# Optimization experiments

Measured on AMD Instinct MI355X. Metric: run time of the kernel, lower is better.

Reference implementation:

```python
import jax, jax.numpy as jnp
import numpy as np
import math

BN, NA, NE = 8192, 15, 16
DO, DA, DE = 96, 88, 80
H, NH = 512, 8
A_MOVE = 6


def _mha(q_in, kv, mask, Wq, Wk, Wv, Wo, n_heads):
    # q_in: [B,H] single query; kv: [B,L,H]; mask: [B,L] bool (True = valid)
    B, Hd = q_in.shape
    Hh = Hd // n_heads
    q = (q_in @ Wq).reshape(B, n_heads, 1, Hh)
    k = (kv @ Wk).reshape(B, -1, n_heads, Hh).transpose(0, 2, 1, 3)  # [B,nh,L,Hh]
    v = (kv @ Wv).reshape(B, -1, n_heads, Hh).transpose(0, 2, 1, 3)
    scores = jnp.einsum('bhqd,bhkd->bhqk', q, k) / math.sqrt(Hh)
    scores = jnp.where(mask[:, None, None, :], scores, -1e9)
    attn = jax.nn.softmax(scores, axis=-1)
    out = jnp.einsum('bhqk,bhkd->bhqd', attn, v).reshape(B, Hd)
    return out @ Wo


def _gru_cell(x, h, W_ih, W_hh, b_ih, b_hh):
    # torch GRU cell math. x: [B,3H], h: [B,H]
    gi = x @ W_ih.T + b_ih  # [B,3H]
    gh = h @ W_hh.T + b_hh  # [B,3H]
    i_r, i_z, i_n = jnp.split(gi, 3, axis=-1)
    h_r, h_z, h_n = jnp.split(gh, 3, axis=-1)
    r = jax.nn.sigmoid(i_r + h_r)
    z = jax.nn.sigmoid(i_z + h_z)
    n = jnp.tanh(i_n + r * h_n)
    return (1.0 - z) * n + z * h


def setup_inputs() -> dict:
    key = jax.random.key(0)
    ks = jax.random.split(key, 24)
    s = 0.02
    inp = {
        'own': jax.random.normal(ks[0], (BN, 1, DO), jnp.float32),
        'ally': jax.random.normal(ks[1], (BN, NA, DA), jnp.float32),
        'enemy': jax.random.normal(ks[2], (BN, NE, DE), jnp.float32),
        'prev_h': jax.random.normal(ks[3], (BN, H), jnp.float32),
        'W_own': jax.random.normal(ks[4], (DO, H), jnp.float32) * s,
        'b_own': jnp.zeros((H,), jnp.float32),
        'W_ally': jax.random.normal(ks[5], (DA, H), jnp.float32) * s,
        'b_ally': jnp.zeros((H,), jnp.float32),
        'W_enemy': jax.random.normal(ks[6], (DE, H), jnp.float32) * s,
        'b_enemy': jnp.zeros((H,), jnp.float32),
        'Wq_a': jax.random.normal(ks[7], (H, H), jnp.float32) * s,
        'Wk_a': jax.random.normal(ks[8], (H, H), jnp.float32) * s,
        'Wv_a': jax.random.normal(ks[9], (H, H), jnp.float32) * s,
        'Wo_a': jax.random.normal(ks[10], (H, H), jnp.float32) * s,
        'Wq_e': jax.random.normal(ks[11], (H, H), jnp.float32) * s,
        'Wk_e': jax.random.normal(ks[12], (H, H), jnp.float32) * s,
        'Wv_e': jax.random.normal(ks[13], (H, H), jnp.float32) * s,
        'Wo_e': jax.random.normal(ks[14], (H, H), jnp.float32) * s,
        'W_ih': jax.random.normal(ks[15], (3 * H, 3 * H), jnp.float32) * s,
        'W_hh': jax.random.normal(ks[16], (3 * H, H), jnp.float32) * s,
        'b_ih': jnp.zeros((3 * H,), jnp.float32),
        'b_hh': jnp.zeros((3 * H,), jnp.float32),
        'W_q': jax.random.normal(ks[17], (H, A_MOVE + NE), jnp.float32) * s,
        'b_q': jnp.zeros((A_MOVE + NE,), jnp.float32),
    }
    return inp


def reference(own, ally, enemy, prev_h,
              W_own, b_own, W_ally, b_ally, W_enemy, b_enemy,
              Wq_a, Wk_a, Wv_a, Wo_a, Wq_e, Wk_e, Wv_e, Wo_e,
              W_ih, W_hh, b_ih, b_hh, W_q, b_q):
    # masks: entity valid iff not all-zero feature row
    ally_mask = ~jnp.all(ally == 0, axis=-1)    # [B,NA]
    enemy_mask = ~jnp.all(enemy == 0, axis=-1)  # [B,NE]

    e_own = (own @ W_own + b_own)[:, 0, :]      # [B,H]
    A = ally @ W_ally + b_ally                   # [B,NA,H]
    E = enemy @ W_enemy + b_enemy                # [B,NE,H]

    zA = _mha(e_own, A, ally_mask, Wq_a, Wk_a, Wv_a, Wo_a, NH)
    zE = _mha(e_own, E, enemy_mask, Wq_e, Wk_e, Wv_e, Wo_e, NH)

    x = jnp.concatenate([e_own, zA, zE], axis=-1)  # [B,3H]
    h = _gru_cell(x, prev_h, W_ih, W_hh, b_ih, b_hh)
    q = h @ W_q + b_q                              # [B, A_move + NE]
    return q
```

## Files before the change

kernel.cpp:

```cpp
#include <hip/hip_runtime.h>
#include <cstdint>


typedef unsigned short bf16_t;
typedef __attribute__((ext_vector_type(8))) short bf16x8;
typedef __attribute__((ext_vector_type(4))) float f32x4;

__device__ inline float bf2f(bf16_t v) { return __uint_as_float(((unsigned)v) << 16); }
__device__ inline bf16_t f2bf(float x) {
    unsigned u = __float_as_uint(x);
    u += 0x7fffu + ((u >> 16) & 1u);
    return (bf16_t)(u >> 16);
}
__device__ inline void gload16(const bf16_t* g, bf16_t* l) {
    __builtin_amdgcn_global_load_lds(
        (const __attribute__((address_space(1))) void*)g,
        (__attribute__((address_space(3))) void*)l, 16, 0, 0);
}
__device__ inline int imin(int a, int b) { return a < b ? a : b; }

struct CJob { const float* s; bf16_t* d; int n4; };
template <int NJ> struct CJobs { CJob j[NJ]; };

template <int NJ>
__global__ __launch_bounds__(256)
void cvt_plain(CJobs<NJ> T)
{
    CJob jb = T.j[blockIdx.y];
    int stride = gridDim.x * 256;
    for (int i = blockIdx.x * 256 + threadIdx.x; i < jb.n4; i += stride) {
        float4 v = ((const float4*)jb.s)[i];
        ushort4 u; u.x = f2bf(v.x); u.y = f2bf(v.y); u.z = f2bf(v.z); u.w = f2bf(v.w);
        ((ushort4*)jb.d)[i] = u;
    }
}

struct TJob { const float* s; bf16_t* d; int R, C; };
template <int NJ> struct TJobs { TJob j[NJ]; };

template <int NJ>
__global__ __launch_bounds__(256)
void cvt_trans(TJobs<NJ> T)
{
    TJob jb = T.j[blockIdx.z];
    int c0 = blockIdx.x * 32, r0 = blockIdx.y * 32;
    if (c0 >= jb.C || r0 >= jb.R) return;
    __shared__ float t[32][33];
    int tx = threadIdx.x & 31, ty = threadIdx.x >> 5;
    for (int i = ty; i < 32; i += 8) {
        int r = r0 + i, c = c0 + tx;
        t[i][tx] = (r < jb.R && c < jb.C) ? jb.s[(int64_t)r * jb.C + c] : 0.f;
    }
    __syncthreads();
    for (int i = ty; i < 32; i += 8) {
        int c = c0 + i, r = r0 + tx;
        if (c < jb.C && r < jb.R) jb.d[(int64_t)c * jb.R + r] = f2bf(t[tx][i]);
    }
}

struct MJob { const bf16_t* A; const bf16_t* Bm; const float* bias; bf16_t* C;
              int lda, ldb, ldc, M, N, K, c32; };
template <int NJ> struct MJobs { MJob j[NJ]; };

template <int NJ>
__global__ __launch_bounds__(256)
void mfma_multi(MJobs<NJ> T)
{
    const MJob jb = T.j[blockIdx.z];
    const int m0 = blockIdx.x * 64, n0 = blockIdx.y * 64;
    if (m0 >= jb.M || n0 >= jb.N) return;
    __shared__ bf16_t As[64][32];
    __shared__ bf16_t Bs[64][32];
    const int tid = threadIdx.x;
    const int wv = tid >> 6, lane = tid & 63;
    const int fr = lane & 15, fq = lane >> 4;
    const int wm = (wv & 1) * 32, wn = (wv >> 1) * 32;
    const int lrow = tid >> 2;
    const int sw = ((lrow >> 1) & 3) ^ (tid & 3);
    const int ar = imin(m0 + lrow, jb.M - 1);
    const int br = imin(n0 + lrow, jb.N - 1);
    const bf16_t* gA = jb.A + (int64_t)ar * jb.lda + sw * 8;
    const bf16_t* gB = jb.Bm + (int64_t)br * jb.ldb + sw * 8;
    bf16_t* lA = &As[wv * 16][0];
    bf16_t* lB = &Bs[wv * 16][0];
    f32x4 acc[2][2] = {};
    for (int k0 = 0; k0 < jb.K; k0 += 32) {
        gload16(gA, lA);
        gload16(gB, lB);
        gA += 32; gB += 32;
        __syncthreads();
        bf16x8 aF[2], bF[2];
#pragma unroll
        for (int i = 0; i < 2; ++i) {
            int rw = wm + i * 16 + fr;
            aF[i] = *(const bf16x8*)&As[rw][(fq ^ ((rw >> 1) & 3)) * 8];
            int rn = wn + i * 16 + fr;
            bF[i] = *(const bf16x8*)&Bs[rn][(fq ^ ((rn >> 1) & 3)) * 8];
        }
#pragma unroll
        for (int i = 0; i < 2; ++i)
#pragma unroll
            for (int j = 0; j < 2; ++j)
                acc[i][j] = __builtin_amdgcn_mfma_f32_16x16x32_bf16(aF[i], bF[j], acc[i][j], 0, 0, 0);
        __syncthreads();
    }
#pragma unroll
    for (int j = 0; j < 2; ++j) {
        const int col = n0 + wn + j * 16 + fr;
        if (col >= jb.N) continue;
        const float bv = jb.bias ? jb.bias[col] : 0.f;
#pragma unroll
        for (int i = 0; i < 2; ++i) {
            const int rowb = m0 + wm + i * 16 + fq * 4;
#pragma unroll
            for (int r = 0; r < 4; ++r) {
                const int row = rowb + r;
                if (row >= jb.M) continue;
                const float v = acc[i][j][r] + bv;
                if (jb.c32) ((float*)jb.C)[(int64_t)row * jb.ldc + col] = v;
                else jb.C[(int64_t)row * jb.ldc + col] = f2bf(v);
            }
        }
    }
}

__global__ __launch_bounds__(256)
void mfma_nt(const bf16_t* __restrict__ A, int lda,
             const bf16_t* __restrict__ Bm, int ldb,
             bf16_t* __restrict__ C, int ldc,
             const float* __restrict__ bias, int K)
{
    __shared__ bf16_t As[128][32];
    __shared__ bf16_t Bs[128][32];
    const int tid = threadIdx.x;
    const int wv = tid >> 6, lane = tid & 63;
    const int fr = lane & 15, fq = lane >> 4;
    const int m0 = blockIdx.x * 128, n0 = blockIdx.y * 128;
    const int wm = (wv & 1) * 64, wn = (wv >> 1) * 64;
    const int lrow = tid >> 2;
    const int sw = ((lrow >> 1) & 3) ^ (tid & 3);
    f32x4 acc[4][4] = {};
    const bf16_t* gA = A + (int64_t)(m0 + lrow) * lda + sw * 8;
    const bf16_t* gB = Bm + (int64_t)(n0 + lrow) * ldb + sw * 8;
    bf16_t* lA0 = &As[wv * 16][0];
    bf16_t* lA1 = &As[64 + wv * 16][0];
    bf16_t* lB0 = &Bs[wv * 16][0];
    bf16_t* lB1 = &Bs[64 + wv * 16][0];
    const int64_t a64 = (int64_t)64 * lda, b64 = (int64_t)64 * ldb;
    for (int k0 = 0; k0 < K; k0 += 32) {
        gload16(gA, lA0);
        gload16(gA + a64, lA1);
        gload16(gB, lB0);
        gload16(gB + b64, lB1);
        gA += 32; gB += 32;
        __syncthreads();
        bf16x8 aF[4], bF[4];
#pragma unroll
        for (int i = 0; i < 4; ++i) {
            int rw = wm + i * 16 + fr;
            aF[i] = *(const bf16x8*)&As[rw][(fq ^ ((rw >> 1) & 3)) * 8];
            int rn = wn + i * 16 + fr;
            bF[i] = *(const bf16x8*)&Bs[rn][(fq ^ ((rn >> 1) & 3)) * 8];
        }
#pragma unroll
        for (int i = 0; i < 4; ++i)
#pragma unroll
            for (int j = 0; j < 4; ++j)
                acc[i][j] = __builtin_amdgcn_mfma_f32_16x16x32_bf16(aF[i], bF[j], acc[i][j], 0, 0, 0);
        __syncthreads();
    }
#pragma unroll
    for (int j = 0; j < 4; ++j) {
        const int col = n0 + wn + j * 16 + fr;
        const float bv = bias[col];
#pragma unroll
        for (int i = 0; i < 4; ++i) {
            const int row = m0 + wm + i * 16 + fq * 4;
#pragma unroll
            for (int r = 0; r < 4; ++r)
                C[(int64_t)(row + r) * ldc + col] = f2bf(acc[i][j][r] + bv);
        }
    }
}

template <int NENT, int DF, int OFF, bool COPYOWN>
__global__ __launch_bounds__(256)
void attn_mfma(const float* __restrict__ ent, const bf16_t* __restrict__ Kq,
               const bf16_t* __restrict__ ownB, bf16_t* __restrict__ acat)
{
    __shared__ bf16_t sent[4][16][104];
    __shared__ bf16_t sentT[4][96][24];
    __shared__ bf16_t pbuf[4][16][24];
    __shared__ float  maskf[4][16];

    const int wv = threadIdx.x >> 6, lane = threadIdx.x & 63;
    const int b = blockIdx.x * 4 + wv;
    const int fr = lane & 15, g = lane >> 4;
    const bf16x8 z8 = {0, 0, 0, 0, 0, 0, 0, 0};

    if (lane < 16) maskf[wv][lane] = -1e9f;
    const float* eb = ent + (int64_t)b * NENT * DF;
#pragma unroll
    for (int t = 0; t < 3; ++t) {
        int idx = lane + t * 64;
        int i = idx / 12, c0 = (idx % 12) * 8;
        float v[8];
        bool data = (i < NENT) && (c0 < DF);
        if (data) {
            float4 a = *(const float4*)(eb + (int64_t)i * DF + c0);
            float4 c = *(const float4*)(eb + (int64_t)i * DF + c0 + 4);
            v[0] = a.x; v[1] = a.y; v[2] = a.z; v[3] = a.w;
            v[4] = c.x; v[5] = c.y; v[6] = c.z; v[7] = c.w;
        } else {
#pragma unroll
            for (int j = 0; j < 8; ++j) v[j] = 0.f;
        }
        bf16x8 pk;
        bool any = false;
#pragma unroll
        for (int j = 0; j < 8; ++j) { pk[j] = (short)f2bf(v[j]); any = any || (v[j] != 0.f); }
        *(bf16x8*)&sent[wv][i][c0] = pk;
#pragma unroll
        for (int j = 0; j < 8; ++j) sentT[wv][c0 + j][i] = (bf16_t)pk[j];
        if (any) maskf[wv][i] = 0.f;
    }
    __syncthreads();

    const bf16_t* kqr = Kq + (size_t)b * 768 + fr * 96;
    const float biash = (fr < 8) ? bf2f(kqr[DF]) : 0.f;
    f32x4 S = {};
#pragma unroll
    for (int m = 0; m < 3; ++m) {
        int kc = m * 32 + g * 8;
        bf16x8 af = *(const bf16x8*)&sent[wv][fr][kc];
        bf16x8 kf = (fr < 8) ? *(const bf16x8*)(kqr + kc) : z8;
        S = __builtin_amdgcn_mfma_f32_16x16x32_bf16(af, kf, S, 0, 0, 0);
    }
    float4 mk = *(const float4*)&maskf[wv][g * 4];
    float s0 = (S[0] + biash) * 0.125f + mk.x;
    float s1 = (S[1] + biash) * 0.125f + mk.y;
    float s2 = (S[2] + biash) * 0.125f + mk.z;
    float s3 = (S[3] + biash) * 0.125f + mk.w;
    float mx = fmaxf(fmaxf(s0, s1), fmaxf(s2, s3));
    mx = fmaxf(mx, __shfl_xor(mx, 16, 64));
    mx = fmaxf(mx, __shfl_xor(mx, 32, 64));
    float e0 = __expf(s0 - mx), e1 = __expf(s1 - mx);
    float e2 = __expf(s2 - mx), e3 = __expf(s3 - mx);
    float sum = e0 + e1 + e2 + e3;
    sum += __shfl_xor(sum, 16, 64);
    sum += __shfl_xor(sum, 32, 64);
    float inv = 1.f / sum;
    ushort4 pu;
    pu.x = f2bf(e0 * inv); pu.y = f2bf(e1 * inv);
    pu.z = f2bf(e2 * inv); pu.w = f2bf(e3 * inv);
    *(ushort4*)&pbuf[wv][fr][g * 4] = pu;
    __syncthreads();

    bf16x8 pa = (g < 2) ? *(const bf16x8*)&pbuf[wv][fr][g * 8] : z8;
    f32x4 o[6] = {};
#pragma unroll
    for (int t = 0; t < 6; ++t) {
        bf16x8 bfv = (g < 2) ? *(const bf16x8*)&sentT[wv][t * 16 + fr][g * 8] : z8;
        o[t] = __builtin_amdgcn_mfma_f32_16x16x32_bf16(pa, bfv, o[t], 0, 0, 0);
    }
    bf16_t* ob = &sent[wv][0][0];
    if (g < 2) {
#pragma unroll
        for (int t = 0; t < 6; ++t)
#pragma unroll
            for (int r = 0; r < 4; ++r)
                ob[(g * 4 + r) * 96 + t * 16 + fr] = f2bf(o[t][r]);
    }
    __syncthreads();

    bf16_t* arow = acat + (int64_t)b * 1440;
    if (COPYOWN && lane < 12)
        *(bf16x8*)(arow + lane * 8) = *(const bf16x8*)(ownB + (int64_t)b * 96 + lane * 8);
    constexpr int CH = DF / 8;
    if (lane < 8 * CH) {
        int hh = lane / CH, j = lane % CH;
        *(bf16x8*)(arow + OFF + hh * DF + j * 8) = *(const bf16x8*)&ob[hh * 96 + j * 8];
    }
}

__global__ __launch_bounds__(256)
void bias_fuse(const float* __restrict__ b_own, const float* __restrict__ b_ally,
               const float* __restrict__ b_enemy,
               const float* __restrict__ Wq_a, const float* __restrict__ Wq_e,
               const float* __restrict__ Wk_a, const float* __restrict__ Wv_a,
               const float* __restrict__ Wk_e, const float* __restrict__ Wv_e,
               float* __restrict__ fb)
{
    int job = blockIdx.x;
    int n = blockIdx.y * 64 + (threadIdx.x >> 2), q = threadIdx.x & 3;
    const float* v; const float* W;
    switch (job) {
        case 0: v = b_own;   W = Wq_a; break;
        case 1: v = b_own;   W = Wq_e; break;
        case 2: v = b_ally;  W = Wk_a; break;
        case 3: v = b_ally;  W = Wv_a; break;
        case 4: v = b_enemy; W = Wk_e; break;
        default: v = b_enemy; W = Wv_e; break;
    }
    float s = 0.f;
    for (int h = q * 128; h < q * 128 + 128; ++h)
        s = fmaf(v[h], W[(int64_t)h * 512 + n], s);
    s += __shfl_xor(s, 1);
    s += __shfl_xor(s, 2);
    if (q == 0) fb[job * 512 + n] = s;
}

__global__ __launch_bounds__(256)
void fixups(const float* __restrict__ fb, bf16_t* __restrict__ FkAB, bf16_t* __restrict__ FkEB,
            float* __restrict__ b2f, const float* __restrict__ b_ih,
            const float* __restrict__ b_own, const float* __restrict__ W_ih,
            const bf16_t* __restrict__ WfaB, const bf16_t* __restrict__ WfeB,
            float* __restrict__ biasgi)
{
    int blk = blockIdx.x, t = threadIdx.x;
    if (blk < 2) {
        int i = blk * 256 + t;
        FkAB[88 * 512 + i] = f2bf(fb[2 * 512 + i]);
        FkEB[80 * 512 + i] = f2bf(fb[4 * 512 + i]);
    } else if (blk < 8) {
        int idx = (blk - 2) * 256 + t;
        int side = idx / 768, n = idx - side * 768;
        int z = n / 96, c = n - z * 96;
        float s = 0.f;
        if (c < 92) {
            const bf16_t* Fk = side ? FkEB : FkAB;
            const float* bq = fb + side * 512;
            const float* bk = fb + (side ? 4 : 2) * 512;
            int BROW = side ? 80 : 88;
            for (int d = 0; d < 64; ++d) {
                float kv = (c == BROW) ? bk[z * 64 + d] : bf2f(Fk[c * 512 + z * 64 + d]);
                s = fmaf(bq[z * 64 + d], kv, s);
            }
        }
        b2f[idx] = s;
    } else {
        int j = (blk - 8) * 64 + (t >> 2), q = t & 3;
        float s = 0.f;
        for (int k = q * 128; k < q * 128 + 128; ++k) {
            s = fmaf(b_own[k],        W_ih[(int64_t)j * 1536 + k], s);
            s = fmaf(fb[3 * 512 + k], bf2f(WfaB[j * 512 + k]), s);
            s = fmaf(fb[5 * 512 + k], bf2f(WfeB[j * 512 + k]), s);
        }
        s += __shfl_xor(s, 1);
        s += __shfl_xor(s, 2);
        if (q == 0) biasgi[j] = s + b_ih[j];
    }
}

__global__ __launch_bounds__(256)
void gru_final(const bf16_t* __restrict__ gi, const bf16_t* __restrict__ gh,
               const float* __restrict__ ph, const bf16_t* __restrict__ Wq,
               const float* __restrict__ bq, float* __restrict__ out, int B)
{
    const int b = blockIdx.x, tid = threadIdx.x;
    __shared__ float sh[512];
    const bf16_t* gib = gi + (int64_t)b * 1536;
    const bf16_t* ghb = gh + (int64_t)b * 1536;
    const float* phb = ph + (int64_t)b * 512;
    for (int n = tid; n < 512; n += 256) {
        float r = 1.f / (1.f + expf(-(bf2f(gib[n]) + bf2f(ghb[n]))));
        float z = 1.f / (1.f + expf(-(bf2f(gib[512 + n]) + bf2f(ghb[512 + n]))));
        float nn = tanhf(bf2f(gib[1024 + n]) + r * bf2f(ghb[1024 + n]));
        sh[n] = (1.f - z) * nn + z * phb[n];
    }
    __syncthreads();
    if (tid < 176) {
        int j = tid >> 3, l = tid & 7;
        float s = 0.f;
        for (int k = l; k < 512; k += 8) s = fmaf(sh[k], bf2f(Wq[j * 512 + k]), s);
        s += __shfl_down(s, 4, 64);
        s += __shfl_down(s, 2, 64);
        s += __shfl_down(s, 1, 64);
        if (l == 0) out[(int64_t)b * 22 + j] = s + bq[j];
    }
}

extern "C" void kernel_launch(void* const* d_in, const int* in_sizes, int n_in,
                              void* d_out, int out_size, void* d_ws, size_t ws_size,
                              hipStream_t stream)
{
    const float* own    = (const float*)d_in[0];
    const float* ally   = (const float*)d_in[1];
    const float* enemy  = (const float*)d_in[2];
    const float* prev_h = (const float*)d_in[3];
    const float* W_own  = (const float*)d_in[4];
    const float* b_own  = (const float*)d_in[5];
    const float* W_ally = (const float*)d_in[6];
    const float* b_ally = (const float*)d_in[7];
    const float* W_enemy= (const float*)d_in[8];
    const float* b_enemy= (const float*)d_in[9];
    const float* Wq_a   = (const float*)d_in[10];
    const float* Wk_a   = (const float*)d_in[11];
    const float* Wv_a   = (const float*)d_in[12];
    const float* Wo_a   = (const float*)d_in[13];
    const float* Wq_e   = (const float*)d_in[14];
    const float* Wk_e   = (const float*)d_in[15];
    const float* Wv_e   = (const float*)d_in[16];
    const float* Wo_e   = (const float*)d_in[17];
    const float* W_ih   = (const float*)d_in[18];
    const float* W_hh   = (const float*)d_in[19];
    const float* b_ih   = (const float*)d_in[20];
    const float* b_hh   = (const float*)d_in[21];
    const float* W_q    = (const float*)d_in[22];
    const float* b_q    = (const float*)d_in[23];
    float* outq = (float*)d_out;
    (void)n_in; (void)out_size;

    const int B = in_sizes[0] / 96;

    float* w = (float*)d_ws;
    size_t o = 0;
    auto alloc = [&](size_t n) { float* p = w + o; o += (n + 3) & ~(size_t)3; return p; };
    bf16_t* WqT[6];
    for (int i = 0; i < 6; ++i) WqT[i] = (bf16_t*)alloc(131072);
    bf16_t* WoaB  = (bf16_t*)alloc(131072);
    bf16_t* WoeB  = (bf16_t*)alloc(131072);
    bf16_t* WihB  = (bf16_t*)alloc(1179648);
    bf16_t* WhhB  = (bf16_t*)alloc(393216);
    bf16_t* WownB = (bf16_t*)alloc(24576);
    bf16_t* WallyB= (bf16_t*)alloc(22528);
    bf16_t* WenemyB=(bf16_t*)alloc(20480);
    bf16_t* ownB  = (bf16_t*)alloc(393216);
    bf16_t* FqaB  = (bf16_t*)alloc(24576);
    bf16_t* FqeB  = (bf16_t*)alloc(24576);
    bf16_t* FkAB  = (bf16_t*)alloc(23552);
    bf16_t* FkEB  = (bf16_t*)alloc(23552);
    bf16_t* FvAB  = (bf16_t*)alloc(22528);
    bf16_t* FvEB  = (bf16_t*)alloc(20480);
    bf16_t* WfaB  = (bf16_t*)alloc(393216);
    bf16_t* WfeB  = (bf16_t*)alloc(393216);
    bf16_t* MmPa  = (bf16_t*)alloc(36864);
    bf16_t* MmPe  = (bf16_t*)alloc(36864);
    float*  b2f   = alloc(1536);
    float*  fb    = alloc(3072);
    bf16_t* Kq    = (bf16_t*)alloc((size_t)B * 768 / 2);
    bf16_t* prevhB= (bf16_t*)w;
    bf16_t* gi    = (bf16_t*)w;
    if (o < (size_t)B * 1536 / 2) return;
    float*  biasgi= alloc(1536);
    bf16_t* WqTq  = (bf16_t*)alloc(5632);
    bf16_t* UTb   = (bf16_t*)alloc(1105920);
    bf16_t* A_cat = (bf16_t*)alloc((size_t)B * 1440 / 2);
    bf16_t* ghB   = (bf16_t*)alloc((size_t)B * 1536 / 2);

    if (ws_size < o * sizeof(float)) return;

    {
        CJobs<8> T;
        T.j[0] = { W_ih,    WihB,    589824 };
        T.j[1] = { W_hh,    WhhB,    196608 };
        T.j[2] = { Wo_a,    WoaB,     65536 };
        T.j[3] = { Wo_e,    WoeB,     65536 };
        T.j[4] = { W_own,   WownB,    12288 };
        T.j[5] = { W_ally,  WallyB,   11264 };
        T.j[6] = { W_enemy, WenemyB,  10240 };
        T.j[7] = { own,     ownB,    196608 };
        hipLaunchKernelGGL((cvt_plain<8>), dim3(128, 8), dim3(256), 0, stream, T);
    }
    {
        TJobs<7> T;
        T.j[0] = { Wq_a, WqT[0], 512, 512 };
        T.j[1] = { Wq_e, WqT[1], 512, 512 };
        T.j[2] = { Wk_a, WqT[2], 512, 512 };
        T.j[3] = { Wk_e, WqT[3], 512, 512 };
        T.j[4] = { Wv_a, WqT[4], 512, 512 };
        T.j[5] = { Wv_e, WqT[5], 512, 512 };
        T.j[6] = { W_q,  WqTq,   512,  22 };
        hipLaunchKernelGGL((cvt_trans<7>), dim3(16, 16, 7), dim3(256), 0, stream, T);
    }
    hipLaunchKernelGGL(bias_fuse, dim3(6, 8), dim3(256), 0, stream,
                       b_own, b_ally, b_enemy, Wq_a, Wq_e, Wk_a, Wv_a, Wk_e, Wv_e, fb);
    {
        MJobs<8> T;
        T.j[0] = { WownB,        WqT[0], nullptr, FqaB, 512, 512, 512,   96, 512, 512, 0 };
        T.j[1] = { WownB,        WqT[1], nullptr, FqeB, 512, 512, 512,   96, 512, 512, 0 };
        T.j[2] = { WallyB,       WqT[2], nullptr, FkAB, 512, 512, 512,   88, 512, 512, 0 };
        T.j[3] = { WenemyB,      WqT[3], nullptr, FkEB, 512, 512, 512,   80, 512, 512, 0 };
        T.j[4] = { WallyB,       WqT[4], nullptr, FvAB, 512, 512, 512,   88, 512, 512, 0 };
        T.j[5] = { WenemyB,      WqT[5], nullptr, FvEB, 512, 512, 512,   80, 512, 512, 0 };
        T.j[6] = { WihB + 512,   WoaB,   nullptr, WfaB, 1536, 512, 512, 1536, 512, 512, 0 };
        T.j[7] = { WihB + 1024,  WoeB,   nullptr, WfeB, 1536, 512, 512, 1536, 512, 512, 0 };
        hipLaunchKernelGGL((mfma_multi<8>), dim3(24, 8, 8), dim3(256), 0, stream, T);
    }
    hipLaunchKernelGGL(fixups, dim3(32), dim3(256), 0, stream,
                       fb, FkAB, FkEB, b2f, b_ih, b_own, W_ih, WfaB, WfeB, biasgi);
    {
        MJobs<33> T;
        for (int h = 0; h < 8; ++h) {
            T.j[h]     = { FkAB + h * 64, FqaB + h * 64, nullptr, MmPa + h * 9216,
                           512, 512, 96, 92, 96, 64, 0 };
            T.j[8 + h] = { FkEB + h * 64, FqeB + h * 64, nullptr, MmPe + h * 9216,
                           512, 512, 96, 92, 96, 64, 0 };
        }
        T.j[16] = { WihB, WownB, nullptr, UTb, 1536, 512, 1440, 1536, 96, 512, 0 };
        for (int h = 0; h < 8; ++h) {
            T.j[17 + h] = { WfaB + h * 64, FvAB + h * 64, nullptr, UTb + 96 + h * 88,
                            512, 512, 1440, 1536, 88, 64, 0 };
            T.j[25 + h] = { WfeB + h * 64, FvEB + h * 64, nullptr, UTb + 800 + h * 80,
                            512, 512, 1440, 1536, 80, 64, 0 };
        }
        hipLaunchKernelGGL((mfma_multi<33>), dim3(24, 2, 33), dim3(256), 0, stream, T);
    }
    {
        CJobs<1> T;
        T.j[0] = { prev_h, prevhB, B * 512 / 4 };
        hipLaunchKernelGGL((cvt_plain<1>), dim3(512, 1), dim3(256), 0, stream, T);
    }
    hipLaunchKernelGGL(mfma_nt, dim3(B / 128, 12), dim3(256), 0, stream,
                       prevhB, 512, WhhB, 512, ghB, 1536, b_hh, 512);
    hipLaunchKernelGGL(mfma_nt, dim3(B / 128, 6), dim3(256), 0, stream,
                       ownB, 96, MmPa, 96, Kq, 768, b2f, 96);
    hipLaunchKernelGGL((attn_mfma<15, 88, 96, true>), dim3(B / 4), dim3(256), 0, stream,
                       ally, Kq, ownB, A_cat);
    hipLaunchKernelGGL(mfma_nt, dim3(B / 128, 6), dim3(256), 0, stream,
                       ownB, 96, MmPe, 96, Kq, 768, b2f + 768, 96);
    hipLaunchKernelGGL((attn_mfma<16, 80, 800, false>), dim3(B / 4), dim3(256), 0, stream,
                       enemy, Kq, ownB, A_cat);
    hipLaunchKernelGGL(mfma_nt, dim3(B / 128, 12), dim3(256), 0, stream,
                       A_cat, 1440, UTb, 1440, gi, 1536, biasgi, 1440);
    hipLaunchKernelGGL(gru_final, dim3(B), dim3(256), 0, stream,
                       gi, ghB, prev_h, WqTq, b_q, outq, B);
}
```

Baseline: 403.1 us.

## Merge prep kernels, stage GEMM epilogue through LDS, vectorize GRU gate loads

```diff
diff --git a/kernel.cpp b/kernel.cpp
--- a/kernel.cpp
+++ b/kernel.cpp
@@ -7,6 +7,8 @@
 typedef __attribute__((ext_vector_type(4))) float f32x4;
 
 __device__ inline float bf2f(bf16_t v) { return __uint_as_float(((unsigned)v) << 16); }
+__device__ inline float bf2f_lo(unsigned u) { return __uint_as_float(u << 16); }
+__device__ inline float bf2f_hi(unsigned u) { return __uint_as_float(u & 0xffff0000u); }
 __device__ inline bf16_t f2bf(float x) {
     unsigned u = __float_as_uint(x);
     u += 0x7fffu + ((u >> 16) & 1u);
@@ -20,41 +22,62 @@
 __device__ inline int imin(int a, int b) { return a < b ? a : b; }
 
 struct CJob { const float* s; bf16_t* d; int n4; };
-template <int NJ> struct CJobs { CJob j[NJ]; };
-
-template <int NJ>
+struct TJob { const float* s; bf16_t* d; int R, C; };
+struct PrepArgs {
+    CJob cj[9];
+    TJob tj[7];
+    const float *b_own, *b_ally, *b_enemy;
+    const float *Wq_a, *Wq_e, *Wk_a, *Wv_a, *Wk_e, *Wv_e;
+    float* fb;
+};
+
 __global__ __launch_bounds__(256)
-void cvt_plain(CJobs<NJ> T)
-{
-    CJob jb = T.j[blockIdx.y];
-    int stride = gridDim.x * 256;
-    for (int i = blockIdx.x * 256 + threadIdx.x; i < jb.n4; i += stride) {
-        float4 v = ((const float4*)jb.s)[i];
-        ushort4 u; u.x = f2bf(v.x); u.y = f2bf(v.y); u.z = f2bf(v.z); u.w = f2bf(v.w);
-        ((ushort4*)jb.d)[i] = u;
-    }
-}
-
-struct TJob { const float* s; bf16_t* d; int R, C; };
-template <int NJ> struct TJobs { TJob j[NJ]; };
-
-template <int NJ>
-__global__ __launch_bounds__(256)
-void cvt_trans(TJobs<NJ> T)
-{
-    TJob jb = T.j[blockIdx.z];
-    int c0 = blockIdx.x * 32, r0 = blockIdx.y * 32;
-    if (c0 >= jb.C || r0 >= jb.R) return;
-    __shared__ float t[32][33];
-    int tx = threadIdx.x & 31, ty = threadIdx.x >> 5;
-    for (int i = ty; i < 32; i += 8) {
-        int r = r0 + i, c = c0 + tx;
-        t[i][tx] = (r < jb.R && c < jb.C) ? jb.s[(int64_t)r * jb.C + c] : 0.f;
-    }
-    __syncthreads();
-    for (int i = ty; i < 32; i += 8) {
-        int c = c0 + i, r = r0 + tx;
-        if (c < jb.C && r < jb.R) jb.d[(int64_t)c * jb.R + r] = f2bf(t[tx][i]);
+void prep(PrepArgs P)
+{
+    const int z = blockIdx.z;
+    if (z < 9) {
+        CJob jb = P.cj[z];
+        int flat = blockIdx.y * 16 + blockIdx.x;
+        for (int i = flat * 256 + threadIdx.x; i < jb.n4; i += 256 * 256) {
+            float4 v = ((const float4*)jb.s)[i];
+            ushort4 u; u.x = f2bf(v.x); u.y = f2bf(v.y); u.z = f2bf(v.z); u.w = f2bf(v.w);
+            ((ushort4*)jb.d)[i] = u;
+        }
+    } else if (z < 16) {
+        TJob jb = P.tj[z - 9];
+        int c0 = blockIdx.x * 32, r0 = blockIdx.y * 32;
+        if (c0 >= jb.C || r0 >= jb.R) return;
+        __shared__ float t[32][33];
+        int tx = threadIdx.x & 31, ty = threadIdx.x >> 5;
+        for (int i = ty; i < 32; i += 8) {
+            int r = r0 + i, c = c0 + tx;
+            t[i][tx] = (r < jb.R && c < jb.C) ? jb.s[(int64_t)r * jb.C + c] : 0.f;
+        }
+        __syncthreads();
+        for (int i = ty; i < 32; i += 8) {
+            int c = c0 + i, r = r0 + tx;
+            if (c < jb.C && r < jb.R) jb.d[(int64_t)c * jb.R + r] = f2bf(t[tx][i]);
+        }
+    } else {
+        int flat = blockIdx.y * 16 + blockIdx.x;
+        if (flat >= 48) return;
+        int job = flat >> 3;
+        int n = (flat & 7) * 64 + (threadIdx.x >> 2), q = threadIdx.x & 3;
+        const float* v; const float* W;
+        switch (job) {
+            case 0: v = P.b_own;   W = P.Wq_a; break;
+            case 1: v = P.b_own;   W = P.Wq_e; break;
+            case 2: v = P.b_ally;  W = P.Wk_a; break;
+            case 3: v = P.b_ally;  W = P.Wv_a; break;
+            case 4: v = P.b_enemy; W = P.Wk_e; break;
+            default: v = P.b_enemy; W = P.Wv_e; break;
+        }
+        float s = 0.f;
+        for (int h = q * 128; h < q * 128 + 128; ++h)
+            s = fmaf(v[h], W[(int64_t)h * 512 + n], s);
+        s += __shfl_xor(s, 1);
+        s += __shfl_xor(s, 2);
+        if (q == 0) P.fb[job * 512 + n] = s;
     }
 }
 
@@ -132,6 +155,7 @@
 {
     __shared__ bf16_t As[128][32];
     __shared__ bf16_t Bs[128][32];
+    __shared__ bf16_t Cs[128][132];
     const int tid = threadIdx.x;
     const int wv = tid >> 6, lane = tid & 63;
     const int fr = lane & 15, fq = lane >> 4;
@@ -171,15 +195,22 @@
     }
 #pragma unroll
     for (int j = 0; j < 4; ++j) {
-        const int col = n0 + wn + j * 16 + fr;
-        const float bv = bias[col];
+        const int col = wn + j * 16 + fr;
+        const float bv = bias[n0 + col];
 #pragma unroll
         for (int i = 0; i < 4; ++i) {
-            const int row = m0 + wm + i * 16 + fq * 4;
+            const int rowb = wm + i * 16 + fq * 4;
 #pragma unroll
             for (int r = 0; r < 4; ++r)
-                C[(int64_t)(row + r) * ldc + col] = f2bf(acc[i][j][r] + bv);
-        }
+                Cs[rowb + r][col] = f2bf(acc[i][j][r] + bv);
+        }
+    }
+    __syncthreads();
+    const int srow = tid >> 4, c8 = (tid & 15) * 8;
+#pragma unroll
+    for (int p = 0; p < 8; ++p) {
+        const int row = srow + p * 16;
+        *(bf16x8*)(C + (int64_t)(m0 + row) * ldc + n0 + c8) = *(const bf16x8*)&Cs[row][c8];
     }
 }
 
@@ -284,33 +315,6 @@
 }
 
 __global__ __launch_bounds__(256)
-void bias_fuse(const float* __restrict__ b_own, const float* __restrict__ b_ally,
-               const float* __restrict__ b_enemy,
-               const float* __restrict__ Wq_a, const float* __restrict__ Wq_e,
-               const float* __restrict__ Wk_a, const float* __restrict__ Wv_a,
-               const float* __restrict__ Wk_e, const float* __restrict__ Wv_e,
-               float* __restrict__ fb)
-{
-    int job = blockIdx.x;
-    int n = blockIdx.y * 64 + (threadIdx.x >> 2), q = threadIdx.x & 3;
-    const float* v; const float* W;
-    switch (job) {
-        case 0: v = b_own;   W = Wq_a; break;
-        case 1: v = b_own;   W = Wq_e; break;
-        case 2: v = b_ally;  W = Wk_a; break;
-        case 3: v = b_ally;  W = Wv_a; break;
-        case 4: v = b_enemy; W = Wk_e; break;
-        default: v = b_enemy; W = Wv_e; break;
-    }
-    float s = 0.f;
-    for (int h = q * 128; h < q * 128 + 128; ++h)
-        s = fmaf(v[h], W[(int64_t)h * 512 + n], s);
-    s += __shfl_xor(s, 1);
-    s += __shfl_xor(s, 2);
-    if (q == 0) fb[job * 512 + n] = s;
-}
-
-__global__ __launch_bounds__(256)
 void fixups(const float* __restrict__ fb, bf16_t* __restrict__ FkAB, bf16_t* __restrict__ FkEB,
             float* __restrict__ b2f, const float* __restrict__ b_ih,
             const float* __restrict__ b_own, const float* __restrict__ W_ih,
@@ -362,11 +366,27 @@
     const bf16_t* gib = gi + (int64_t)b * 1536;
     const bf16_t* ghb = gh + (int64_t)b * 1536;
     const float* phb = ph + (int64_t)b * 512;
-    for (int n = tid; n < 512; n += 256) {
-        float r = 1.f / (1.f + expf(-(bf2f(gib[n]) + bf2f(ghb[n]))));
-        float z = 1.f / (1.f + expf(-(bf2f(gib[512 + n]) + bf2f(ghb[512 + n]))));
-        float nn = tanhf(bf2f(gib[1024 + n]) + r * bf2f(ghb[1024 + n]));
-        sh[n] = (1.f - z) * nn + z * phb[n];
+    {
+        const int n = tid * 2;
+        unsigned gr = *(const unsigned*)(gib + n);
+        unsigned gz = *(const unsigned*)(gib + 512 + n);
+        unsigned gn = *(const unsigned*)(gib + 1024 + n);
+        unsigned hr = *(const unsigned*)(ghb + n);
+        unsigned hz = *(const unsigned*)(ghb + 512 + n);
+        unsigned hn = *(const unsigned*)(ghb + 1024 + n);
+        float2 p2 = *(const float2*)(phb + n);
+        {
+            float r = 1.f / (1.f + __expf(-(bf2f_lo(gr) + bf2f_lo(hr))));
+            float z = 1.f / (1.f + __expf(-(bf2f_lo(gz) + bf2f_lo(hz))));
+            float nn = tanhf(bf2f_lo(gn) + r * bf2f_lo(hn));
+            sh[n] = (1.f - z) * nn + z * p2.x;
+        }
+        {
+            float r = 1.f / (1.f + __expf(-(bf2f_hi(gr) + bf2f_hi(hr))));
+            float z = 1.f / (1.f + __expf(-(bf2f_hi(gz) + bf2f_hi(hz))));
+            float nn = tanhf(bf2f_hi(gn) + r * bf2f_hi(hn));
+            sh[n + 1] = (1.f - z) * nn + z * p2.y;
+        }
     }
     __syncthreads();
     if (tid < 176) {
@@ -439,7 +459,6 @@
     float*  b2f   = alloc(1536);
     float*  fb    = alloc(3072);
     bf16_t* Kq    = (bf16_t*)alloc((size_t)B * 768 / 2);
-    bf16_t* prevhB= (bf16_t*)w;
     bf16_t* gi    = (bf16_t*)w;
     if (o < (size_t)B * 1536 / 2) return;
     float*  biasgi= alloc(1536);
@@ -447,34 +466,35 @@
     bf16_t* UTb   = (bf16_t*)alloc(1105920);
     bf16_t* A_cat = (bf16_t*)alloc((size_t)B * 1440 / 2);
     bf16_t* ghB   = (bf16_t*)alloc((size_t)B * 1536 / 2);
+    bf16_t* prevhB= (bf16_t*)alloc((size_t)B * 512 / 2);
 
     if (ws_size < o * sizeof(float)) return;
 
     {
-        CJobs<8> T;
-        T.j[0] = { W_ih,    WihB,    589824 };
-        T.j[1] = { W_hh,    WhhB,    196608 };
-        T.j[2] = { Wo_a,    WoaB,     65536 };
-        T.j[3] = { Wo_e,    WoeB,     65536 };
-        T.j[4] = { W_own,   WownB,    12288 };
-        T.j[5] = { W_ally,  WallyB,   11264 };
-        T.j[6] = { W_enemy, WenemyB,  10240 };
-        T.j[7] = { own,     ownB,    196608 };
-        hipLaunchKernelGGL((cvt_plain<8>), dim3(128, 8), dim3(256), 0, stream, T);
-    }
-    {
-        TJobs<7> T;
-        T.j[0] = { Wq_a, WqT[0], 512, 512 };
-        T.j[1] = { Wq_e, WqT[1], 512, 512 };
-        T.j[2] = { Wk_a, WqT[2], 512, 512 };
-        T.j[3] = { Wk_e, WqT[3], 512, 512 };
-        T.j[4] = { Wv_a, WqT[4], 512, 512 };
-        T.j[5] = { Wv_e, WqT[5], 512, 512 };
-        T.j[6] = { W_q,  WqTq,   512,  22 };
-        hipLaunchKernelGGL((cvt_trans<7>), dim3(16, 16, 7), dim3(256), 0, stream, T);
-    }
-    hipLaunchKernelGGL(bias_fuse, dim3(6, 8), dim3(256), 0, stream,
-                       b_own, b_ally, b_enemy, Wq_a, Wq_e, Wk_a, Wv_a, Wk_e, Wv_e, fb);
+        PrepArgs P;
+        P.cj[0] = { W_ih,    WihB,    589824 };
+        P.cj[1] = { W_hh,    WhhB,    196608 };
+        P.cj[2] = { Wo_a,    WoaB,     65536 };
+        P.cj[3] = { Wo_e,    WoeB,     65536 };
+        P.cj[4] = { W_own,   WownB,    12288 };
+        P.cj[5] = { W_ally,  WallyB,   11264 };
+        P.cj[6] = { W_enemy, WenemyB,  10240 };
+        P.cj[7] = { own,     ownB,    196608 };
+        P.cj[8] = { prev_h,  prevhB,  B * 512 / 4 };
+        P.tj[0] = { Wq_a, WqT[0], 512, 512 };
+        P.tj[1] = { Wq_e, WqT[1], 512, 512 };
+        P.tj[2] = { Wk_a, WqT[2], 512, 512 };
+        P.tj[3] = { Wk_e, WqT[3], 512, 512 };
+        P.tj[4] = { Wv_a, WqT[4], 512, 512 };
+        P.tj[5] = { Wv_e, WqT[5], 512, 512 };
+        P.tj[6] = { W_q,  WqTq,   512,  22 };
+        P.b_own = b_own; P.b_ally = b_ally; P.b_enemy = b_enemy;
+        P.Wq_a = Wq_a; P.Wq_e = Wq_e; P.Wk_a = Wk_a; P.Wv_a = Wv_a;
+        P.Wk_e = Wk_e; P.Wv_e = Wv_e; P.fb = fb;
+        hipLaunchKernelGGL(prep, dim3(16, 16, 17), dim3(256), 0, stream, P);
+    }
+    hipLaunchKernelGGL(mfma_nt, dim3(B / 128, 12), dim3(256), 0, stream,
+                       prevhB, 512, WhhB, 512, ghB, 1536, b_hh, 512);
     {
         MJobs<8> T;
         T.j[0] = { WownB,        WqT[0], nullptr, FqaB, 512, 512, 512,   96, 512, 512, 0 };
@@ -506,13 +526,6 @@
         }
         hipLaunchKernelGGL((mfma_multi<33>), dim3(24, 2, 33), dim3(256), 0, stream, T);
     }
-    {
-        CJobs<1> T;
-        T.j[0] = { prev_h, prevhB, B * 512 / 4 };
-        hipLaunchKernelGGL((cvt_plain<1>), dim3(512, 1), dim3(256), 0, stream, T);
-    }
-    hipLaunchKernelGGL(mfma_nt, dim3(B / 128, 12), dim3(256), 0, stream,
-                       prevhB, 512, WhhB, 512, ghB, 1536, b_hh, 512);
     hipLaunchKernelGGL(mfma_nt, dim3(B / 128, 6), dim3(256), 0, stream,
                        ownB, 96, MmPa, 96, Kq, 768, b2f, 96);
     hipLaunchKernelGGL((attn_mfma<15, 88, 96, true>), dim3(B / 4), dim3(256), 0, stream,
```

Result: faster. 381.2 us (-5.4%).
